# Kernel optimization log

Measured on AMD Instinct MI355X. Metric: run time of the kernel, lower is better.

## Reference

```python
import jax, jax.numpy as jnp
import numpy as np

N, B, E, D, DQ, H = 20000, 32, 320000, 128, 1024, 2
L = N // B  # 625 nodes per graph (equal-size graphs -> static max_node_num)
NUM_GNN_LAYERS = 3


def setup_inputs() -> dict:
    key = jax.random.key(0)
    ks = jax.random.split(key, 32)
    rn = lambda k, s, scale=1.0: jax.random.normal(k, s, jnp.float32) * scale
    w = lambda k, fi, fo: rn(k, (fi, fo), 1.0 / np.sqrt(fi))
    inp = {
        'x': rn(ks[0], (N, D)),
        'edge_attr': rn(ks[1], (E, D)),
        'u': rn(ks[2], (B, D)),
        'qa_attr': rn(ks[3], (B, DQ)),
        # edge MLP: cat(src,dest,edge_attr,u[eb]) = 4D -> hidden D -> D
        'W_e1': w(ks[4], 4 * D, D), 'b_e1': jnp.zeros((D,)),
        'W_e2': w(ks[5], D, D), 'b_e2': jnp.zeros((D,)),
        # weight mlp: cat(edge_attr, u[eb]) = 2D -> 1 (num_layers=1)
        'W_w': w(ks[6], 2 * D, 1), 'b_w': jnp.zeros((1,)),
        # message mlp: cat(x[row], edge_attr) = 2D -> D -> D
        'W_m1': w(ks[7], 2 * D, D), 'b_m1': jnp.zeros((D,)),
        'W_m2': w(ks[8], D, D), 'b_m2': jnp.zeros((D,)),
        # update mlp: cat(x, received, u[nb]) = 3D -> D -> D
        'W_u1': w(ks[9], 3 * D, D), 'b_u1': jnp.zeros((D,)),
        'W_u2': w(ks[10], D, D), 'b_u2': jnp.zeros((D,)),
        # multihead att-pool: q from qa_attr (DQ) -> H*dk; k,v from evidence (D) -> H*dk
        'W_q': w(ks[11], DQ, D), 'b_q': jnp.zeros((D,)),
        'W_k': w(ks[12], D, D), 'b_k': jnp.zeros((D,)),
        'W_v': w(ks[13], D, D), 'b_v': jnp.zeros((D,)),
        'edge_index': jax.random.randint(ks[14], (2, E), 0, N, dtype=jnp.int32),
        'node_batch': (jnp.arange(N, dtype=jnp.int32) // L).astype(jnp.int32),
        'num_of_nodes': jnp.full((B,), L, dtype=jnp.int32),
    }
    return inp


def _mlp2(h, W1, b1, W2, b2):
    return jax.nn.relu(h @ W1 + b1) @ W2 + b2


def _seg_softmax(logits, seg, num):
    m = jax.ops.segment_max(logits, seg, num_segments=num)
    e = jnp.exp(logits - m[seg])
    s = jax.ops.segment_sum(e, seg, num_segments=num)
    return e / s[seg]


def reference(x, edge_attr, u, qa_attr,
              W_e1, b_e1, W_e2, b_e2, W_w, b_w,
              W_m1, b_m1, W_m2, b_m2, W_u1, b_u1, W_u2, b_u2,
              W_q, b_q, W_k, b_k, W_v, b_v,
              edge_index, node_batch, num_of_nodes):
    row, col = edge_index[0], edge_index[1]
    edge_batch = node_batch[row]
    Bsz, Nn = u.shape[0], x.shape[0]
    Lm = Nn // Bsz  # static max_node_num (equal-size graphs)

    norm_w = None
    for _ in range(NUM_GNN_LAYERS):
        ue = u[edge_batch]  # [E, D]
        # EdgeModel: cat(src, dest, edge_attr, u[eb]) -> MLP -> new edge_attr
        new_edge = _mlp2(jnp.concatenate([x[row], x[col], edge_attr, ue], 1),
                         W_e1, b_e1, W_e2, b_e2)
        # edge weights from OLD edge_attr (per EdgeV1Model.forward)
        wts = jnp.concatenate([edge_attr, ue], 1) @ W_w + b_w  # [E,1]
        norm_w = _seg_softmax(wts[:, 0], edge_batch, Bsz)[:, None]  # [E,1]
        edge_attr = new_edge
        # NodeModel: message MLP, weighted scatter_mean over col, update MLP
        msg = _mlp2(jnp.concatenate([x[row], edge_attr], 1), W_m1, b_m1, W_m2, b_m2)
        summed = jax.ops.segment_sum(msg * norm_w, col, num_segments=Nn)
        cnt = jax.ops.segment_sum(jnp.ones((msg.shape[0],), msg.dtype), col, num_segments=Nn)
        received = summed / jnp.maximum(cnt, 1.0)[:, None]
        x = _mlp2(jnp.concatenate([x, received, u[node_batch]], 1),
                  W_u1, b_u1, W_u2, b_u2)

    pooled_edge = jax.ops.segment_sum(edge_attr * norm_w, edge_batch, num_segments=Bsz)  # [B,D]
    # evidence packing: equal graphs -> simple reshape, then exact GELU
    evidence = jax.nn.gelu(x.reshape(Bsz, Lm, -1), approximate=False)  # [B,L,D]
    mask = jnp.arange(Lm)[None, :] >= num_of_nodes[:, None]  # [B,L] True = masked

    # MultiheadAttPoolLayer
    dk = W_k.shape[1] // H
    q = (qa_attr @ W_q + b_q).reshape(Bsz, H, dk)
    k = (evidence @ W_k + b_k).reshape(Bsz, Lm, H, dk)
    v = (evidence @ W_v + b_v).reshape(Bsz, Lm, H, dk)
    scores = jnp.einsum('bhd,blhd->bhl', q, k) / jnp.sqrt(jnp.float32(dk))
    scores = jnp.where(mask[:, None, :], -1e30, scores)
    attn = jax.nn.softmax(scores, axis=-1)
    pooled_node = jnp.einsum('bhl,blhd->bhd', attn, v).reshape(Bsz, H * dk)  # [B,D]

    return jnp.concatenate([pooled_edge, pooled_node], 1)  # [B, 2D]
```

## Files before the change

### kernel.cpp

```cpp
#include <hip/hip_runtime.h>
#include <math.h>

typedef __bf16 bf16_t;
typedef bf16_t bf16x8 __attribute__((ext_vector_type(8)));
typedef bf16_t bf16x4 __attribute__((ext_vector_type(4)));
typedef bf16_t bf16x2 __attribute__((ext_vector_type(2)));
typedef float  f32x4  __attribute__((ext_vector_type(4)));

#define N_NODES 20000
#define NEDGE   320000
#define DIM     128
#define TP      136
#define EBLK    2500
#define FWAVES  10000
#define NBLK    625
#define GPRE    157
#define PBLK    512

#define FE1  0
#define FCE  49152
#define FM1  65536
#define FCM  81920
#define FU1  114688
#define FU2  163840
#define FK   180224
#define FV   196608
#define FWC  212992
#define WF_ELEMS 229376

__device__ __forceinline__ void acc_zero32(f32x4 acc[2][8]) {
  f32x4 z = {0.f, 0.f, 0.f, 0.f};
#pragma unroll
  for (int i = 0; i < 2; ++i)
#pragma unroll
    for (int j = 0; j < 8; ++j) acc[i][j] = z;
}

__device__ __forceinline__ void wstage_rows_bf(bf16_t* sA, const bf16_t* src, int rowreg, int lane) {
  int r = lane >> 1, h = lane & 1;
  int row = __shfl(rowreg, r);
  const bf16_t* sp = src + (size_t)row * DIM + h * 64;
  bf16_t* dp = sA + r * TP + h * 64;
#pragma unroll
  for (int i = 0; i < 8; ++i)
    *(uint4*)(dp + i * 8) = *(const uint4*)(sp + i * 8);
}

__device__ __forceinline__ void wstage_rows_f32(bf16_t* sA, const float* src, int rowreg, int lane) {
  int r = lane >> 1, h = lane & 1;
  int row = __shfl(rowreg, r);
  const float* sp = src + (size_t)row * DIM + h * 64;
  bf16_t* dp = sA + r * TP + h * 64;
#pragma unroll
  for (int i = 0; i < 8; ++i) {
    float4 f0 = *(const float4*)(sp + i * 8);
    float4 f1 = *(const float4*)(sp + i * 8 + 4);
    bf16x8 tv;
    tv[0]=(bf16_t)f0.x; tv[1]=(bf16_t)f0.y; tv[2]=(bf16_t)f0.z; tv[3]=(bf16_t)f0.w;
    tv[4]=(bf16_t)f1.x; tv[5]=(bf16_t)f1.y; tv[6]=(bf16_t)f1.z; tv[7]=(bf16_t)f1.w;
    *(bf16x8*)(dp + i * 8) = tv;
  }
}

__device__ __forceinline__ void wstage_seq_bf(bf16_t* sA, const bf16_t* src, int base, int lane) {
  int r = lane >> 1, h = lane & 1;
  const bf16_t* sp = src + (size_t)(base + r) * DIM + h * 64;
  bf16_t* dp = sA + r * TP + h * 64;
#pragma unroll
  for (int i = 0; i < 8; ++i)
    *(uint4*)(dp + i * 8) = *(const uint4*)(sp + i * 8);
}

__device__ __forceinline__ void wstage_seq_f32(bf16_t* sA, const float* src, int base, int lane) {
  int r = lane >> 1, h = lane & 1;
  const float* sp = src + (size_t)(base + r) * DIM + h * 64;
  bf16_t* dp = sA + r * TP + h * 64;
#pragma unroll
  for (int i = 0; i < 8; ++i) {
    float4 f0 = *(const float4*)(sp + i * 8);
    float4 f1 = *(const float4*)(sp + i * 8 + 4);
    bf16x8 tv;
    tv[0]=(bf16_t)f0.x; tv[1]=(bf16_t)f0.y; tv[2]=(bf16_t)f0.z; tv[3]=(bf16_t)f0.w;
    tv[4]=(bf16_t)f1.x; tv[5]=(bf16_t)f1.y; tv[6]=(bf16_t)f1.z; tv[7]=(bf16_t)f1.w;
    *(bf16x8*)(dp + i * 8) = tv;
  }
}

__device__ __forceinline__ void chunk_stage(bf16_t* ch, const bf16_t* __restrict__ src, int t) {
#pragma unroll
  for (int i = 0; i < 8; ++i) {
    int idx = (i * 256 + t) * 8;
    *(uint4*)(ch + idx) = *(const uint4*)(src + idx);
  }
}

__device__ __forceinline__ void wmfma_lds(const bf16_t* sA, const bf16_t* ch,
                                          int lane, int lm, int lq, f32x4 acc[2][8]) {
#pragma unroll
  for (int kk = 0; kk < 4; ++kk) {
    int ko = kk * 32 + lq * 8;
    bf16x8 a0 = *(const bf16x8*)(sA + lm * TP + ko);
    bf16x8 a1 = *(const bf16x8*)(sA + (16 + lm) * TP + ko);
    const bf16_t* wp = ch + (kk << 12) + (lane << 3);
#pragma unroll
    for (int ct = 0; ct < 8; ++ct) {
      bf16x8 bfr = *(const bf16x8*)(wp + (ct << 9));
      acc[0][ct] = __builtin_amdgcn_mfma_f32_16x16x32_bf16(a0, bfr, acc[0][ct], 0, 0, 0);
      acc[1][ct] = __builtin_amdgcn_mfma_f32_16x16x32_bf16(a1, bfr, acc[1][ct], 0, 0, 0);
    }
  }
}

__device__ __forceinline__ void wmfma_gk128(const bf16_t* sA, const bf16_t* __restrict__ Wf,
                                            int lane, int lm, int lq, f32x4 acc[2][8]) {
#pragma unroll
  for (int kk = 0; kk < 4; ++kk) {
    int ko = kk * 32 + lq * 8;
    bf16x8 a0 = *(const bf16x8*)(sA + lm * TP + ko);
    bf16x8 a1 = *(const bf16x8*)(sA + (16 + lm) * TP + ko);
    const bf16_t* wp = Wf + ((kk * 8) << 9) + (lane << 3);
#pragma unroll
    for (int ct = 0; ct < 8; ++ct) {
      bf16x8 bfr = *(const bf16x8*)(wp + (ct << 9));
      acc[0][ct] = __builtin_amdgcn_mfma_f32_16x16x32_bf16(a0, bfr, acc[0][ct], 0, 0, 0);
      acc[1][ct] = __builtin_amdgcn_mfma_f32_16x16x32_bf16(a1, bfr, acc[1][ct], 0, 0, 0);
    }
  }
}

__device__ __forceinline__ void merge_shfl(float& m, float& s, int width) {
  for (int k = 1; k < width; k <<= 1) {
    float m2 = __shfl_xor(m, k), s2 = __shfl_xor(s, k);
    float M = fmaxf(m, m2), ns = 0.f;
    if (m  > -1e29f) ns += s  * expf(m  - M);
    if (m2 > -1e29f) ns += s2 * expf(m2 - M);
    m = M; s = ns;
  }
}

__global__ void gn_xcvt(const float* x, bf16_t* xb) {
  int i = blockIdx.x * 256 + threadIdx.x;
  if (i < N_NODES * DIM / 4) {
    float4 f = ((const float4*)x)[i];
    bf16x4 o; o[0]=(bf16_t)f.x; o[1]=(bf16_t)f.y; o[2]=(bf16_t)f.z; o[3]=(bf16_t)f.w;
    *(bf16x4*)(xb + (size_t)i * 4) = o;
  }
}

__global__ void gn_wcomb(const float* Wm2, const float* Wu1, const float* We2,
                         const float* We1, const float* Wm1,
                         float* wc1, float* wce, float* wcm) {
  int idx = blockIdx.x * 256 + threadIdx.x;
  if (idx >= 16384) return;
  int i = idx >> 7, j = idx & 127;
  float acc = 0.f;
  if (blockIdx.y == 0) {
    for (int m = 0; m < 128; ++m) acc += Wm2[i * 128 + m] * Wu1[(128 + m) * 128 + j];
    wc1[idx] = acc;
  } else if (blockIdx.y == 1) {
    for (int m = 0; m < 128; ++m) acc += We2[i * 128 + m] * We1[(256 + m) * 128 + j];
    wce[idx] = acc;
  } else {
    for (int m = 0; m < 128; ++m) acc += We2[i * 128 + m] * Wm1[(128 + m) * 128 + j];
    wcm[idx] = acc;
  }
}

__global__ void gn_fragw(const float* We1, const float* Wce, const float* Wm1, const float* Wcm,
                         const float* Wm2, const float* Wu1, const float* Wu2,
                         const float* Wk, const float* Wv, const float* Wc1, bf16_t* WF) {
  int idx = blockIdx.x * 256 + threadIdx.x;
  if (idx >= WF_ELEMS) return;
  int seg = idx >> 14;
  const float* W; int kc;
  switch (seg) {
    case 0:  W = We1; kc = 0; break;
    case 1:  W = We1; kc = 1; break;
    case 2:  W = We1; kc = 2; break;
    case 3:  W = Wce; kc = 0; break;
    case 4:  W = Wm1; kc = 0; break;
    case 5:  W = Wcm; kc = 0; break;
    case 6:  W = Wm2; kc = 0; break;
    case 7:  W = Wu1; kc = 0; break;
    case 8:  W = Wu1; kc = 1; break;
    case 9:  W = Wu1; kc = 2; break;
    case 10: W = Wu2; kc = 0; break;
    case 11: W = Wk;  kc = 0; break;
    case 12: W = Wv;  kc = 0; break;
    default: W = Wc1; kc = 0; break;
  }
  int r = idx & 16383;
  int j = r & 7, lane = (r >> 3) & 63, ct = (r >> 9) & 7, kk = (r >> 12) & 3;
  int k = kc * 128 + kk * 32 + (lane >> 4) * 8 + j;
  int n = ct * 16 + (lane & 15);
  WF[idx] = (bf16_t)W[k * 128 + n];
}

__global__ void gn_uprep(const float* u, const float* We1, const float* be1,
                         const float* Ww, const float* bw,
                         const float* bm2, const float* Wu1,
                         const float* bm1, const float* be2,
                         const float* Wm1, const float* We2,
                         float* Rp0, float* Rp12, float* uw, float* uw2,
                         float* bm2u, float* bm1p, float* wv) {
  int t = threadIdx.x;
  for (int idx = blockIdx.x * 256 + t; idx < 32 * 128; idx += gridDim.x * 256) {
    int g = idx >> 7, c = idx & 127;
    float acc = be1[c];
    for (int k = 0; k < 128; ++k) acc += u[g * 128 + k] * We1[(384 + k) * 128 + c];
    float be12 = 0.f;
    for (int k = 0; k < 128; ++k) be12 += be2[k] * We1[(256 + k) * 128 + c];
    int tc = g * 128 + (c & 15) * 8 + (c >> 4);
    Rp0[tc] = acc;
    Rp12[tc] = acc + be12;
  }
  if (blockIdx.x == 0 && t < 32) {
    float acc = bw[0];
    for (int k = 0; k < 128; ++k) acc += u[t * 128 + k] * Ww[128 + k];
    float bsh = 0.f;
    for (int c = 0; c < 128; ++c) bsh += be2[c] * Ww[c];
    uw[t] = acc;
    uw2[t] = acc + bsh;
  }
  if (blockIdx.x == 1 && t < 128) {
    float a1 = 0.f, a2 = 0.f, a3 = 0.f;
    for (int k = 0; k < 128; ++k) {
      a1 += bm2[k] * Wu1[(128 + k) * 128 + t];
      a2 += be2[k] * Wm1[(128 + k) * 128 + t];
      a3 += We2[t * 128 + k] * Ww[k];
    }
    bm2u[t] = a1;
    bm1p[t] = bm1[t] + a2;
    wv[t] = a3;
  }
}

__global__ void gn_counti(const int* ei, int* cnti) {
  int e = blockIdx.x * 256 + threadIdx.x;
  if (e < NEDGE) atomicAdd(&cnti[ei[NEDGE + e]], 1);
}

__global__ void gn_scan(const int* cnti, int* off, int* curs) {
  __shared__ int part[256];
  int t = threadIdx.x;
  int base = t * 80;
  int lim = base + 80; if (lim > N_NODES) lim = N_NODES;
  int s = 0;
  for (int i = base; i < lim; ++i) s += cnti[i];
  part[t] = s;
  __syncthreads();
  for (int d = 1; d < 256; d <<= 1) {
    int add = (t >= d) ? part[t - d] : 0;
    __syncthreads();
    part[t] += add;
    __syncthreads();
  }
  int pfx = (t == 0) ? 0 : part[t - 1];
  for (int i = base; i < lim; ++i) {
    off[i] = pfx; curs[i] = pfx; pfx += cnti[i];
  }
  if (t == 0) off[N_NODES] = NEDGE;
}

__global__ void gn_eidx(const int* ei, int* curs, int* eidx) {
  int e = blockIdx.x * 256 + threadIdx.x;
  if (e < NEDGE) {
    int c = ei[NEDGE + e];
    int pos = atomicAdd(&curs[c], 1);
    eidx[pos] = e;
  }
}

__global__ void gn_q(const float* qa, const float* Wq, const float* bq, float* qb) {
  int b = blockIdx.x, t = threadIdx.x;
  int c = t & 127, half = t >> 7;
  const float* qrow = qa + b * 1024 + half * 512;
  float acc = 0.f;
  for (int k = 0; k < 512; ++k) acc += qrow[k] * Wq[(half * 512 + k) * 128 + c];
  __shared__ float red[256];
  red[t] = acc;
  __syncthreads();
  if (half == 0) qb[b * 128 + c] = red[c] + red[128 + c] + bq[c];
}

__global__ void gn_wl0(const float* ea, const float* Ww, const float* uw,
                       const int* ei, const int* nbat, float* wl, int* gb) {
  int t = threadIdx.x;
  int sub = t & 15, grp = t >> 4;
  for (int e = blockIdx.x * 16 + grp; e < NEDGE; e += gridDim.x * 16) {
    const float* er = ea + (size_t)e * DIM + sub * 8;
    float s = 0.f;
#pragma unroll
    for (int j = 0; j < 8; ++j) s += er[j] * Ww[sub * 8 + j];
#pragma unroll
    for (int m = 1; m < 16; m <<= 1) s += __shfl_xor(s, m);
    if (sub == 0) {
      int g = nbat[ei[e]];
      wl[e] = s + uw[g];
      gb[e] = g;
    }
  }
}

__global__ void gn_part0(const float* wl, const int* gb, float* pm, float* ps) {
  __shared__ float lv[128];
  __shared__ int   lgg[128];
  int t = threadIdx.x, blk = blockIdx.x, e0 = blk * 128;
  if (t < 128) { lv[t] = wl[e0 + t]; lgg[t] = gb[e0 + t]; }
  __syncthreads();
  int g = t >> 3, seg = t & 7;
  float m = -1e30f, s = 0.f;
  for (int i = seg * 16; i < seg * 16 + 16; ++i)
    if (lgg[i] == g) {
      float v = lv[i];
      if (v > m) { s = s * expf(m - v) + 1.f; m = v; }
      else s += expf(v - m);
    }
  merge_shfl(m, s, 8);
  if (seg == 0) { pm[g * FWAVES + blk] = m; ps[g * FWAVES + blk] = s; }
}

__global__ void gn_reduce_ms(const float* pm, const float* ps, float* mg, float* sg, int nb) {
  int g = blockIdx.x, t = threadIdx.x;
  __shared__ float red[256];
  float m = -1e30f;
  for (int i = t; i < nb; i += 256) m = fmaxf(m, pm[g * FWAVES + i]);
  red[t] = m; __syncthreads();
  for (int s2 = 128; s2 > 0; s2 >>= 1) { if (t < s2) red[t] = fmaxf(red[t], red[t + s2]); __syncthreads(); }
  m = red[0]; __syncthreads();
  float s = 0.f;
  for (int i = t; i < nb; i += 256) {
    float sb = ps[g * FWAVES + i];
    if (sb > 0.f) s += sb * expf(pm[g * FWAVES + i] - m);
  }
  red[t] = s; __syncthreads();
  for (int s2 = 128; s2 > 0; s2 >>= 1) { if (t < s2) red[t] += red[t + s2]; __syncthreads(); }
  if (t == 0) { mg[g] = m; sg[g] = red[0]; }
}

__global__ __launch_bounds__(256, 2) void gn_fused(
    const bf16_t* __restrict__ xb,
    const void* esrcv, int efirst,
    bf16_t* edst,
    const bf16_t* __restrict__ WF,
    const float* Rp, const float* UW2, const float* wv, const float* bm1p,
    const float* wl_cur, const float* mg, const float* sg,
    float* wl_next, float* pm, float* ps, int last,
    const int* ei, const int* gb, bf16_t* msg,
    const float* uu, const float* bu1, const int* nbat, float* pre,
    float* nwout) {
  __shared__ bf16_t chunk[16384];
  __shared__ bf16_t band[4][32 * TP];
  __shared__ float slwt[128];

  int t = threadIdx.x;
  int w = t >> 6, lane = t & 63;
  int lm = lane & 15, lq = lane >> 4;
  int blk = blockIdx.x;
  bf16_t* myband = band[w];

  if (blk >= EBLK) {
    int nb128 = blk - EBLK;
    int gb32 = nb128 * 4 + w;
    int lrow = 0, lgr = 0;
    if (lane < 32) {
      int node = gb32 * 32 + lane;
      if (node > N_NODES - 1) node = N_NODES - 1;
      lrow = node;
      lgr = nbat[node];
    }
    f32x4 acc[2][8];
    acc_zero32(acc);
    wstage_rows_bf(myband, xb, lrow, lane);
    chunk_stage(chunk, WF + FU1, t);
    __syncthreads();
    wmfma_lds(myband, chunk, lane, lm, lq, acc);
    __syncthreads();
    wstage_rows_f32(myband, uu, lgr, lane);
    chunk_stage(chunk, WF + FU1 + 32768, t);
    __syncthreads();
    wmfma_lds(myband, chunk, lane, lm, lq, acc);
    if (gb32 < NBLK) {
      float* pp = pre + (size_t)gb32 * 4096 + lane;
#pragma unroll
      for (int rt = 0; rt < 2; ++rt)
#pragma unroll
        for (int reg = 0; reg < 4; ++reg)
#pragma unroll
          for (int ct = 0; ct < 8; ++ct)
            pp[((rt * 32 + reg * 8 + ct) << 6)] = acc[rt][ct][reg] + bu1[ct * 16 + lm];
    }
    return;
  }

  int e0 = blk * 128;
  int ew0 = e0 + w * 32;
  int lrowr = 0, lcolr = 0, lgr = 0;
  float lnwr = 0.f;
  if (lane < 32) {
    int e = ew0 + lane;
    lrowr = ei[e];
    lcolr = ei[NEDGE + e];
    lgr = gb[e];
    lnwr = expf(wl_cur[e] - mg[lgr]) / sg[lgr];
    nwout[e] = lnwr;
  }

  f32x4 accE[2][8], accM[2][8];
  acc_zero32(accE);
  acc_zero32(accM);

  uint4 c0, c1, c2, c3, c4, c5, c6, c7;
#define CLOAD(SRC) { const uint4* _s = (const uint4*)(SRC) + t; \
  c0 = _s[0];    c1 = _s[256];  c2 = _s[512];  c3 = _s[768]; \
  c4 = _s[1024]; c5 = _s[1280]; c6 = _s[1536]; c7 = _s[1792]; }
#define CWRITE() { uint4* _d = (uint4*)chunk + t; \
  _d[0] = c0;    _d[256] = c1;  _d[512] = c2;  _d[768] = c3; \
  _d[1024] = c4; _d[1280] = c5; _d[1536] = c6; _d[1792] = c7; }

  CLOAD(WF + FE1);
  wstage_rows_bf(myband, xb, lrowr, lane);
  CWRITE();
  __syncthreads();

  CLOAD(WF + FM1);
  wmfma_lds(myband, chunk, lane, lm, lq, accE);
  __syncthreads();
  CWRITE();
  __syncthreads();

  CLOAD(WF + FE1 + 16384);
  wmfma_lds(myband, chunk, lane, lm, lq, accM);
  wstage_rows_bf(myband, xb, lcolr, lane);
  __syncthreads();
  CWRITE();
  __syncthreads();

  CLOAD(efirst ? (WF + FE1 + 32768) : (WF + FCE));
  wmfma_lds(myband, chunk, lane, lm, lq, accE);
  if (efirst) wstage_seq_f32(myband, (const float*)esrcv, ew0, lane);
  else        wstage_seq_bf (myband, (const bf16_t*)esrcv, ew0, lane);
  __syncthreads();
  CWRITE();
  __syncthreads();

  CLOAD(WF + FCM);
  wmfma_lds(myband, chunk, lane, lm, lq, accE);
  {
    float ww8[8];
#pragma unroll
    for (int ct = 0; ct < 8; ++ct) ww8[ct] = wv[ct * 16 + lm];
#pragma unroll
    for (int rt = 0; rt < 2; ++rt)
#pragma unroll
      for (int reg = 0; reg < 4; ++reg) {
        int row = rt * 16 + lq * 4 + reg;
        int g = __shfl(lgr, row);
        const float4* rp = (const float4*)(Rp + (size_t)g * 128 + lm * 8);
        float4 ra = rp[0], rb = rp[1];
        float rv[8] = {ra.x, ra.y, ra.z, ra.w, rb.x, rb.y, rb.z, rb.w};
        float lsum = 0.f;
#pragma unroll
        for (int ct = 0; ct < 8; ++ct) {
          int col = ct * 16 + lm;
          float v = fmaxf(accE[rt][ct][reg] + rv[ct], 0.f);
          myband[row * TP + col] = (bf16_t)v;
          lsum += v * ww8[ct];
        }
        if (!last) {
          lsum += __shfl_xor(lsum, 1);
          lsum += __shfl_xor(lsum, 2);
          lsum += __shfl_xor(lsum, 4);
          lsum += __shfl_xor(lsum, 8);
          if (lm == 0) {
            float v2 = lsum + UW2[g];
            wl_next[ew0 + row] = v2;
            slwt[w * 32 + row] = v2;
          }
        }
      }
    int r = lane >> 1, h = lane & 1;
    bf16_t* dp = edst + (size_t)(ew0 + r) * DIM + h * 64;
    const bf16_t* sp2 = myband + r * TP + h * 64;
#pragma unroll
    for (int i = 0; i < 8; ++i)
      *(uint4*)(dp + i * 8) = *(const uint4*)(sp2 + i * 8);
  }
  __syncthreads();
  CWRITE();
  __syncthreads();

  wmfma_lds(myband, chunk, lane, lm, lq, accM);
  {
    float bm18[8];
#pragma unroll
    for (int ct = 0; ct < 8; ++ct) bm18[ct] = bm1p[ct * 16 + lm];
#pragma unroll
    for (int rt = 0; rt < 2; ++rt)
#pragma unroll
      for (int reg = 0; reg < 4; ++reg) {
        int row = rt * 16 + lq * 4 + reg;
        float nwv = __shfl(lnwr, row);
#pragma unroll
        for (int ct = 0; ct < 8; ++ct) {
          int col = ct * 16 + lm;
          myband[row * TP + col] = (bf16_t)(fmaxf(accM[rt][ct][reg] + bm18[ct], 0.f) * nwv);
        }
      }
    int r = lane >> 1, h = lane & 1;
    bf16_t* dp = msg + (size_t)(ew0 + r) * DIM + h * 64;
    const bf16_t* sp2 = myband + r * TP + h * 64;
#pragma unroll
    for (int i = 0; i < 8; ++i)
      *(uint4*)(dp + i * 8) = *(const uint4*)(sp2 + i * 8);
  }

  if (!last) {
    int g = lane >> 1, seg = lane & 1;
    float m = -1e30f, s = 0.f;
    for (int i = seg * 16; i < seg * 16 + 16; ++i) {
      int gi = __shfl(lgr, i);
      if (gi == g) {
        float v = slwt[w * 32 + i];
        if (v > m) { s = s * expf(m - v) + 1.f; m = v; }
        else s += expf(v - m);
      }
    }
    merge_shfl(m, s, 2);
    if (seg == 0) { pm[g * FWAVES + blk * 4 + w] = m; ps[g * FWAVES + blk * 4 + w] = s; }
  }
#undef CLOAD
#undef CWRITE
}

__global__ __launch_bounds__(256) void gn_gather(
    const bf16_t* __restrict__ msg, const float* __restrict__ nw,
    const int* __restrict__ off, const int* __restrict__ eidx,
    bf16_t* recvb, float* rnw) {
  int w = threadIdx.x >> 6, lane = threadIdx.x & 63;
  int n = blockIdx.x * 4 + w;
  int o0 = off[n], o1 = off[n + 1];
  float a0 = 0.f, a1 = 0.f, snw = 0.f;
  int i = o0;
  for (; i + 3 < o1; i += 4) {
    int e0 = eidx[i], e1 = eidx[i + 1], e2 = eidx[i + 2], e3 = eidx[i + 3];
    bf16x2 v0 = *(const bf16x2*)(msg + (size_t)e0 * DIM + lane * 2);
    bf16x2 v1 = *(const bf16x2*)(msg + (size_t)e1 * DIM + lane * 2);
    bf16x2 v2 = *(const bf16x2*)(msg + (size_t)e2 * DIM + lane * 2);
    bf16x2 v3 = *(const bf16x2*)(msg + (size_t)e3 * DIM + lane * 2);
    a0 += (float)v0[0] + (float)v1[0] + (float)v2[0] + (float)v3[0];
    a1 += (float)v0[1] + (float)v1[1] + (float)v2[1] + (float)v3[1];
    snw += nw[e0] + nw[e1] + nw[e2] + nw[e3];
  }
  for (; i < o1; ++i) {
    int e = eidx[i];
    bf16x2 v = *(const bf16x2*)(msg + (size_t)e * DIM + lane * 2);
    a0 += (float)v[0];
    a1 += (float)v[1];
    snw += nw[e];
  }
  float ic = 1.f / fmaxf((float)(o1 - o0), 1.f);
  bf16x2 o; o[0] = (bf16_t)(a0 * ic); o[1] = (bf16_t)(a1 * ic);
  *(bf16x2*)(recvb + (size_t)n * DIM + lane * 2) = o;
  if (lane == 0) rnw[n] = snw * ic;
}

__global__ __launch_bounds__(64, 3) void gn_node(
    bf16_t* xdst, const bf16_t* recvb, const float* rnw, const float* pre,
    const bf16_t* __restrict__ WF, const float* bu2, const float* bm2u) {
  __shared__ bf16_t sA[32 * TP];

  int lane = threadIdx.x;
  int nb = blockIdx.x;
  int n0 = nb * 32;
  int lm = lane & 15, lq = lane >> 4;

  float rnwreg = 0.f;
  if (lane < 32) rnwreg = rnw[n0 + lane];

  wstage_seq_bf(sA, recvb, n0, lane);

  f32x4 acc[2][8];
  acc_zero32(acc);
  wmfma_gk128(sA, WF + FWC, lane, lm, lq, acc);

  const float* pp = pre + (size_t)nb * 4096 + lane;
  float bm2u8[8];
#pragma unroll
  for (int ct = 0; ct < 8; ++ct) bm2u8[ct] = bm2u[ct * 16 + lm];
#pragma unroll
  for (int rt = 0; rt < 2; ++rt)
#pragma unroll
    for (int reg = 0; reg < 4; ++reg) {
      int row = rt * 16 + lq * 4 + reg;
      float rv = __shfl(rnwreg, row);
#pragma unroll
      for (int ct = 0; ct < 8; ++ct) {
        int col = ct * 16 + lm;
        sA[row * TP + col] = (bf16_t)fmaxf(
            acc[rt][ct][reg] + rv * bm2u8[ct] + pp[((rt * 32 + reg * 8 + ct) << 6)], 0.f);
      }
    }
  acc_zero32(acc);
  wmfma_gk128(sA, WF + FU2, lane, lm, lq, acc);

  {
    float bu28[8];
#pragma unroll
    for (int ct = 0; ct < 8; ++ct) bu28[ct] = bu2[ct * 16 + lm];
#pragma unroll
    for (int rt = 0; rt < 2; ++rt)
#pragma unroll
      for (int reg = 0; reg < 4; ++reg) {
        int row = rt * 16 + lq * 4 + reg;
        bf16_t* dr = xdst + (size_t)(n0 + row) * DIM;
#pragma unroll
        for (int ct = 0; ct < 8; ++ct) {
          int col = ct * 16 + lm;
          dr[col] = (bf16_t)(acc[rt][ct][reg] + bu28[ct]);
        }
      }
  }
}

__global__ __launch_bounds__(64, 3) void gn_ev(
    const bf16_t* xsrc, const bf16_t* __restrict__ WF,
    const float* bk, const float* bv, float* kb, float* vb) {
  __shared__ bf16_t sA[32 * TP];

  int lane = threadIdx.x;
  int n0 = blockIdx.x * 32;
  int sel = blockIdx.y;
  const bf16_t* Wf = WF + (sel ? FV : FK);
  const float* bias = sel ? bv : bk;
  float* dst = sel ? vb : kb;
  int lm = lane & 15, lq = lane >> 4;

  {
    int r = lane >> 1, h = lane & 1;
    const bf16_t* sp = xsrc + (size_t)(n0 + r) * DIM + h * 64;
    bf16_t* dp = sA + r * TP + h * 64;
#pragma unroll
    for (int i = 0; i < 8; ++i) {
      uint4 v = *(const uint4*)(sp + i * 8);
      bf16_t tmp[8];
      *(uint4*)tmp = v;
      bf16x8 tv;
#pragma unroll
      for (int j = 0; j < 8; ++j) {
        float f = (float)tmp[j];
        tv[j] = (bf16_t)(0.5f * f * (1.f + erff(f * 0.70710678118654752f)));
      }
      *(bf16x8*)(dp + i * 8) = tv;
    }
  }

  f32x4 acc[2][8];
  acc_zero32(acc);
  wmfma_gk128(sA, Wf, lane, lm, lq, acc);

  {
    float b8[8];
#pragma unroll
    for (int ct = 0; ct < 8; ++ct) b8[ct] = bias[ct * 16 + lm];
#pragma unroll
    for (int rt = 0; rt < 2; ++rt)
#pragma unroll
      for (int reg = 0; reg < 4; ++reg) {
        int row = rt * 16 + lq * 4 + reg;
        float* dr = dst + (size_t)(n0 + row) * DIM;
#pragma unroll
        for (int ct = 0; ct < 8; ++ct) {
          int col = ct * 16 + lm;
          dr[col] = acc[rt][ct][reg] + b8[ct];
        }
      }
  }
}

__global__ __launch_bounds__(256, 2) void gn_pooled_edge(
    const bf16_t* __restrict__ he, const float* __restrict__ nw,
    const int* __restrict__ gb, float* pep, float* pepn) {
  __shared__ float loc[4][4096];
  __shared__ float nws[4][32];
  int t = threadIdx.x;
  int lane = t & 63, w = t >> 6;
  float* myloc = loc[w];
  for (int i = lane; i < 4096; i += 64) myloc[i] = 0.f;
  if (lane < 32) nws[w][lane] = 0.f;

  int wid = blockIdx.x * 4 + w;
  int c0 = lane * 2;
  for (int e = wid; e < NEDGE; e += PBLK * 4) {
    int g = gb[e];
    float nwt = nw[e];
    bf16x2 v = *(const bf16x2*)(he + (size_t)e * DIM + c0);
    float* a = myloc + g * 128 + c0;
    float2 cur = *(float2*)a;
    cur.x += (float)v[0] * nwt;
    cur.y += (float)v[1] * nwt;
    *(float2*)a = cur;
    if (lane == 0) nws[w][g] += nwt;
  }
  __syncthreads();
  float* pp = pep + (size_t)blockIdx.x * 4096;
  for (int i = t; i < 4096; i += 256)
    pp[i] = loc[0][i] + loc[1][i] + loc[2][i] + loc[3][i];
  if (t < 32)
    pepn[blockIdx.x * 32 + t] = nws[0][t] + nws[1][t] + nws[2][t] + nws[3][t];
}

__global__ __launch_bounds__(1024) void gn_att(
    const float* qb, const float* kb, const float* vb, const int* non, float* out) {
  int b = blockIdx.x >> 1, h = blockIdx.x & 1, t = threadIdx.x;
  __shared__ float qv[64];
  __shared__ float sc[625];
  __shared__ float red[1024];
  if (t < 64) qv[t] = qb[b * 128 + h * 64 + t];
  __syncthreads();
  int nn = non[b];
  const float4* qv4 = (const float4*)qv;
  for (int l = t; l < 625; l += 1024) {
    float acc = 0.f;
    const float4* kr = (const float4*)(kb + ((size_t)(b * 625 + l)) * DIM + h * 64);
#pragma unroll
    for (int d2 = 0; d2 < 16; ++d2) {
      float4 kv = kr[d2];
      float4 qq = qv4[d2];
      acc += qq.x * kv.x + qq.y * kv.y + qq.z * kv.z + qq.w * kv.w;
    }
    sc[l] = (l < nn) ? acc * 0.125f : -1e30f;
  }
  __syncthreads();
  float m = -1e30f;
  for (int l = t; l < 625; l += 1024) m = fmaxf(m, sc[l]);
  red[t] = m; __syncthreads();
  for (int s2 = 512; s2 > 0; s2 >>= 1) { if (t < s2) red[t] = fmaxf(red[t], red[t + s2]); __syncthreads(); }
  m = red[0]; __syncthreads();
  float ssum = 0.f;
  for (int l = t; l < 625; l += 1024) { float e = expf(sc[l] - m); sc[l] = e; ssum += e; }
  red[t] = ssum; __syncthreads();
  for (int s2 = 512; s2 > 0; s2 >>= 1) { if (t < s2) red[t] += red[t + s2]; __syncthreads(); }
  float inv = 1.f / red[0];
  __syncthreads();
  int d = t & 63, seg = t >> 6;
  float acc = 0.f;
  for (int l = seg; l < 625; l += 16) acc += sc[l] * vb[((size_t)(b * 625 + l)) * DIM + h * 64 + d];
  red[t] = acc; __syncthreads();
  if (t < 64) {
    float v = 0.f;
#pragma unroll
    for (int s = 0; s < 16; ++s) v += red[s * 64 + t];
    out[b * 256 + 128 + h * 64 + d] = v * inv;
  }
}

__global__ void gn_fin1(const float* pep, const float* pepn, float* spool, float* nwg) {
  int i = blockIdx.x * 256 + threadIdx.x;
  float s = 0.f;
#pragma unroll 8
  for (int blk = 0; blk < PBLK; ++blk) s += pep[(size_t)blk * 4096 + i];
  spool[i] = s;
  if (i < 32) {
    float sn = 0.f;
    for (int blk = 0; blk < PBLK; ++blk) sn += pepn[blk * 32 + i];
    nwg[i] = sn;
  }
}

__global__ void gn_fin2(const float* spool, const float* nwg, const float* We2,
                        const float* be2, float* out) {
  int i = blockIdx.x * 256 + threadIdx.x;
  int b = i >> 7, c = i & 127;
  float acc = nwg[b] * be2[c];
  for (int k = 0; k < 128; ++k) acc += spool[b * 128 + k] * We2[k * 128 + c];
  out[b * 256 + c] = acc;
}

extern "C" void kernel_launch(void* const* d_in, const int* in_sizes, int n_in,
                              void* d_out, int out_size, void* d_ws, size_t ws_size,
                              hipStream_t stream) {
  const float* x   = (const float*)d_in[0];
  const float* ea  = (const float*)d_in[1];
  const float* u   = (const float*)d_in[2];
  const float* qa  = (const float*)d_in[3];
  const float* We1 = (const float*)d_in[4];
  const float* be1 = (const float*)d_in[5];
  const float* We2 = (const float*)d_in[6];
  const float* be2 = (const float*)d_in[7];
  const float* Ww  = (const float*)d_in[8];
  const float* bw  = (const float*)d_in[9];
  const float* Wm1 = (const float*)d_in[10];
  const float* bm1 = (const float*)d_in[11];
  const float* Wm2 = (const float*)d_in[12];
  const float* bm2 = (const float*)d_in[13];
  const float* Wu1 = (const float*)d_in[14];
  const float* bu1 = (const float*)d_in[15];
  const float* Wu2 = (const float*)d_in[16];
  const float* bu2 = (const float*)d_in[17];
  const float* Wq  = (const float*)d_in[18];
  const float* bq  = (const float*)d_in[19];
  const float* Wk  = (const float*)d_in[20];
  const float* bk  = (const float*)d_in[21];
  const float* Wv  = (const float*)d_in[22];
  const float* bv  = (const float*)d_in[23];
  const int* ei   = (const int*)d_in[24];
  const int* nbat = (const int*)d_in[25];
  const int* non  = (const int*)d_in[26];
  float* out = (float*)d_out;

  char* p = (char*)d_ws;
  auto alloc = [&](size_t bytes) { char* r = p; p += (bytes + 255) & ~(size_t)255; return r; };
  bf16_t* EB    = (bf16_t*)alloc((size_t)NEDGE * DIM * 2);
  bf16_t* XB    = (bf16_t*)alloc((size_t)N_NODES * DIM * 2);
  bf16_t* XB0   = (bf16_t*)alloc((size_t)N_NODES * DIM * 2);
  bf16_t* MSG   = (bf16_t*)alloc((size_t)NEDGE * DIM * 2);
  bf16_t* RECVB = (bf16_t*)alloc((size_t)N_NODES * DIM * 2);
  int*   CNTI = (int*)alloc((size_t)N_NODES * 4);
  int*   OFF  = (int*)alloc((size_t)(N_NODES + 1) * 4);
  int*   CURS = (int*)alloc((size_t)N_NODES * 4);
  int*   EIDX = (int*)alloc((size_t)NEDGE * 4);
  float* WL   = (float*)alloc((size_t)NEDGE * 4);
  float* WLn  = (float*)alloc((size_t)NEDGE * 4);
  float* NW   = (float*)alloc((size_t)NEDGE * 4);
  float* RNW  = (float*)alloc((size_t)N_NODES * 4);
  int*   GB   = (int*)alloc((size_t)NEDGE * 4);
  float* PM   = (float*)alloc((size_t)32 * FWAVES * 4);
  float* PS   = (float*)alloc((size_t)32 * FWAVES * 4);
  float* MG   = (float*)alloc(32 * 4);
  float* SG   = (float*)alloc(32 * 4);
  float* RP0  = (float*)alloc(32 * 128 * 4);
  float* RP12 = (float*)alloc(32 * 128 * 4);
  float* UW   = (float*)alloc(32 * 4);
  float* UW2  = (float*)alloc(32 * 4);
  float* WC1  = (float*)alloc(16384 * 4);
  float* WCE  = (float*)alloc(16384 * 4);
  float* WCM  = (float*)alloc(16384 * 4);
  float* BM2U = (float*)alloc(128 * 4);
  float* BM1P = (float*)alloc(128 * 4);
  float* WVV  = (float*)alloc(128 * 4);
  bf16_t* WF  = (bf16_t*)alloc((size_t)WF_ELEMS * 2);
  float* QB   = (float*)alloc(32 * 128 * 4);
  float* KB   = (float*)alloc((size_t)N_NODES * DIM * 4);
  float* VB   = (float*)alloc((size_t)N_NODES * DIM * 4);
  float* PEP  = (float*)alloc((size_t)PBLK * 4096 * 4);
  float* PEPN = (float*)alloc((size_t)PBLK * 32 * 4);
  float* SPOOL= (float*)alloc(4096 * 4);
  float* NWG  = (float*)alloc(32 * 4);
  float* PRE  = (float*)alloc((size_t)N_NODES * DIM * 4);

  hipMemsetAsync(CNTI, 0, (size_t)N_NODES * 4, stream);

  gn_xcvt<<<(N_NODES * DIM / 4 + 255) / 256, 256, 0, stream>>>(x, XB0);
  gn_wcomb<<<dim3(64, 3), 256, 0, stream>>>(Wm2, Wu1, We2, We1, Wm1, WC1, WCE, WCM);
  gn_fragw<<<(WF_ELEMS + 255) / 256, 256, 0, stream>>>(We1, WCE, Wm1, WCM, Wm2, Wu1, Wu2, Wk, Wv, WC1, WF);
  gn_uprep<<<16, 256, 0, stream>>>(u, We1, be1, Ww, bw, bm2, Wu1, bm1, be2, Wm1, We2,
                                   RP0, RP12, UW, UW2, BM2U, BM1P, WVV);
  gn_counti<<<1250, 256, 0, stream>>>(ei, CNTI);
  gn_scan<<<1, 256, 0, stream>>>(CNTI, OFF, CURS);
  gn_eidx<<<1250, 256, 0, stream>>>(ei, CURS, EIDX);
  gn_q<<<32, 256, 0, stream>>>(qa, Wq, bq, QB);
  gn_wl0<<<2500, 256, 0, stream>>>(ea, Ww, UW, ei, nbat, WL, GB);
  gn_part0<<<EBLK, 256, 0, stream>>>(WL, GB, PM, PS);

  for (int layer = 0; layer < 3; ++layer) {
    int first = (layer == 0) ? 1 : 0;
    int last = (layer == 2) ? 1 : 0;
    const bf16_t* xs = first ? XB0 : XB;
    const void* es = first ? (const void*)ea : (const void*)EB;
    const float* rp = first ? RP0 : RP12;
    float* cur = (layer == 1) ? WLn : WL;
    float* nxt = (layer == 1) ? WL : WLn;
    gn_reduce_ms<<<32, 256, 0, stream>>>(PM, PS, MG, SG, first ? EBLK : FWAVES);
    gn_fused<<<EBLK + GPRE, 256, 0, stream>>>(xs, es, first, EB, WF, rp, UW2, WVV, BM1P,
                                              cur, MG, SG, nxt, PM, PS, last, ei, GB, MSG,
                                              u, bu1, nbat, PRE, NW);
    gn_gather<<<5000, 256, 0, stream>>>(MSG, NW, OFF, EIDX, RECVB, RNW);
    gn_node<<<NBLK, 64, 0, stream>>>(XB, RECVB, RNW, PRE, WF, bu2, BM2U);
  }

  gn_pooled_edge<<<PBLK, 256, 0, stream>>>(EB, NW, GB, PEP, PEPN);
  gn_ev<<<dim3(NBLK, 2), 64, 0, stream>>>(XB, WF, bk, bv, KB, VB);
  gn_att<<<64, 1024, 0, stream>>>(QB, KB, VB, non, out);
  gn_fin1<<<16, 256, 0, stream>>>(PEP, PEPN, SPOOL, NWG);
  gn_fin2<<<16, 256, 0, stream>>>(SPOOL, NWG, We2, be2, out);
}
```

Baseline: 1.259 ms.

## Widen fused edge kernel to 12 waves per block sharing staged weight chunks

The fused edge/message kernel now runs 768-thread blocks (12 waves, 384 edges) instead of 256-thread blocks. Each staged weight chunk in LDS is therefore shared by three times as many waves, cutting weight-staging traffic per edge. The separate edge and message accumulators are merged into one, with the message MLP moved after the edge MLP, which lowers register pressure enough to allow larger blocks. Smaller changes vectorise the wl0 loads and widen the softmax-stat reduction to 1024 threads. The cost is one resident block per CU, more barrier-heavy synchronisation across 12 waves, and a partial tail block.

```diff
diff --git a/kernel.cpp b/kernel.cpp
--- a/kernel.cpp
+++ b/kernel.cpp
@@ -14,7 +14,9 @@
 #define EBLK    2500
 #define FWAVES  10000
 #define NBLK    625
-#define GPRE    157
+#define EWBLK   384
+#define EBLK2   834
+#define PREB    53
 #define PBLK    512
 
 #define FE1  0
@@ -83,14 +85,6 @@
     tv[0]=(bf16_t)f0.x; tv[1]=(bf16_t)f0.y; tv[2]=(bf16_t)f0.z; tv[3]=(bf16_t)f0.w;
     tv[4]=(bf16_t)f1.x; tv[5]=(bf16_t)f1.y; tv[6]=(bf16_t)f1.z; tv[7]=(bf16_t)f1.w;
     *(bf16x8*)(dp + i * 8) = tv;
-  }
-}
-
-__device__ __forceinline__ void chunk_stage(bf16_t* ch, const bf16_t* __restrict__ src, int t) {
-#pragma unroll
-  for (int i = 0; i < 8; ++i) {
-    int idx = (i * 256 + t) * 8;
-    *(uint4*)(ch + idx) = *(const uint4*)(src + idx);
   }
 }
 
@@ -288,10 +282,11 @@
   int t = threadIdx.x;
   int sub = t & 15, grp = t >> 4;
   for (int e = blockIdx.x * 16 + grp; e < NEDGE; e += gridDim.x * 16) {
-    const float* er = ea + (size_t)e * DIM + sub * 8;
-    float s = 0.f;
-#pragma unroll
-    for (int j = 0; j < 8; ++j) s += er[j] * Ww[sub * 8 + j];
+    const float4* er4 = (const float4*)(ea + (size_t)e * DIM + sub * 8);
+    float4 va = er4[0], vb = er4[1];
+    const float* wp = Ww + sub * 8;
+    float s = va.x * wp[0] + va.y * wp[1] + va.z * wp[2] + va.w * wp[3]
+            + vb.x * wp[4] + vb.y * wp[5] + vb.z * wp[6] + vb.w * wp[7];
 #pragma unroll
     for (int m = 1; m < 16; m <<= 1) s += __shfl_xor(s, m);
     if (sub == 0) {
@@ -320,25 +315,26 @@
   if (seg == 0) { pm[g * FWAVES + blk] = m; ps[g * FWAVES + blk] = s; }
 }
 
-__global__ void gn_reduce_ms(const float* pm, const float* ps, float* mg, float* sg, int nb) {
+__global__ __launch_bounds__(1024) void gn_reduce_ms(
+    const float* pm, const float* ps, float* mg, float* sg, int nb) {
   int g = blockIdx.x, t = threadIdx.x;
-  __shared__ float red[256];
+  __shared__ float red[1024];
   float m = -1e30f;
-  for (int i = t; i < nb; i += 256) m = fmaxf(m, pm[g * FWAVES + i]);
+  for (int i = t; i < nb; i += 1024) m = fmaxf(m, pm[g * FWAVES + i]);
   red[t] = m; __syncthreads();
-  for (int s2 = 128; s2 > 0; s2 >>= 1) { if (t < s2) red[t] = fmaxf(red[t], red[t + s2]); __syncthreads(); }
+  for (int s2 = 512; s2 > 0; s2 >>= 1) { if (t < s2) red[t] = fmaxf(red[t], red[t + s2]); __syncthreads(); }
   m = red[0]; __syncthreads();
   float s = 0.f;
-  for (int i = t; i < nb; i += 256) {
+  for (int i = t; i < nb; i += 1024) {
     float sb = ps[g * FWAVES + i];
     if (sb > 0.f) s += sb * expf(pm[g * FWAVES + i] - m);
   }
   red[t] = s; __syncthreads();
-  for (int s2 = 128; s2 > 0; s2 >>= 1) { if (t < s2) red[t] += red[t + s2]; __syncthreads(); }
+  for (int s2 = 512; s2 > 0; s2 >>= 1) { if (t < s2) red[t] += red[t + s2]; __syncthreads(); }
   if (t == 0) { mg[g] = m; sg[g] = red[0]; }
 }
 
-__global__ __launch_bounds__(256, 2) void gn_fused(
+__global__ __launch_bounds__(768, 1) void gn_fused(
     const bf16_t* __restrict__ xb,
     const void* esrcv, int efirst,
     bf16_t* edst,
@@ -350,8 +346,8 @@
     const float* uu, const float* bu1, const int* nbat, float* pre,
     float* nwout) {
   __shared__ bf16_t chunk[16384];
-  __shared__ bf16_t band[4][32 * TP];
-  __shared__ float slwt[128];
+  __shared__ bf16_t band[12][32 * TP];
+  __shared__ float slwt[384];
 
   int t = threadIdx.x;
   int w = t >> 6, lane = t & 63;
@@ -359,28 +355,37 @@
   int blk = blockIdx.x;
   bf16_t* myband = band[w];
 
-  if (blk >= EBLK) {
-    int nb128 = blk - EBLK;
-    int gb32 = nb128 * 4 + w;
+  uint4 c0, c1, c2, c3;
+#define CLOAD(SRC) if (t < 512) { const uint4* _s = (const uint4*)(SRC) + t; \
+  c0 = _s[0]; c1 = _s[512]; c2 = _s[1024]; c3 = _s[1536]; }
+#define CWRITE() if (t < 512) { uint4* _d = (uint4*)chunk + t; \
+  _d[0] = c0; _d[512] = c1; _d[1024] = c2; _d[1536] = c3; }
+
+  if (blk >= EBLK2) {
+    int gb32 = (blk - EBLK2) * 12 + w;
+    int act = (gb32 < NBLK);
     int lrow = 0, lgr = 0;
-    if (lane < 32) {
+    if (act && lane < 32) {
       int node = gb32 * 32 + lane;
-      if (node > N_NODES - 1) node = N_NODES - 1;
       lrow = node;
       lgr = nbat[node];
     }
     f32x4 acc[2][8];
     acc_zero32(acc);
-    wstage_rows_bf(myband, xb, lrow, lane);
-    chunk_stage(chunk, WF + FU1, t);
+    CLOAD(WF + FU1);
+    if (act) wstage_rows_bf(myband, xb, lrow, lane);
+    CWRITE();
     __syncthreads();
-    wmfma_lds(myband, chunk, lane, lm, lq, acc);
+    CLOAD(WF + FU1 + 32768);
+    if (act) {
+      wmfma_lds(myband, chunk, lane, lm, lq, acc);
+      wstage_rows_f32(myband, uu, lgr, lane);
+    }
     __syncthreads();
-    wstage_rows_f32(myband, uu, lgr, lane);
-    chunk_stage(chunk, WF + FU1 + 32768, t);
+    CWRITE();
     __syncthreads();
-    wmfma_lds(myband, chunk, lane, lm, lq, acc);
-    if (gb32 < NBLK) {
+    if (act) {
+      wmfma_lds(myband, chunk, lane, lm, lq, acc);
       float* pp = pre + (size_t)gb32 * 4096 + lane;
 #pragma unroll
       for (int rt = 0; rt < 2; ++rt)
@@ -393,11 +398,11 @@
     return;
   }
 
-  int e0 = blk * 128;
-  int ew0 = e0 + w * 32;
+  int ew0 = blk * EWBLK + w * 32;
+  int act = (ew0 < NEDGE);
   int lrowr = 0, lcolr = 0, lgr = 0;
   float lnwr = 0.f;
-  if (lane < 32) {
+  if (act && lane < 32) {
     int e = ew0 + lane;
     lrowr = ei[e];
     lcolr = ei[NEDGE + e];
@@ -406,47 +411,36 @@
     nwout[e] = lnwr;
   }
 
-  f32x4 accE[2][8], accM[2][8];
-  acc_zero32(accE);
-  acc_zero32(accM);
-
-  uint4 c0, c1, c2, c3, c4, c5, c6, c7;
-#define CLOAD(SRC) { const uint4* _s = (const uint4*)(SRC) + t; \
-  c0 = _s[0];    c1 = _s[256];  c2 = _s[512];  c3 = _s[768]; \
-  c4 = _s[1024]; c5 = _s[1280]; c6 = _s[1536]; c7 = _s[1792]; }
-#define CWRITE() { uint4* _d = (uint4*)chunk + t; \
-  _d[0] = c0;    _d[256] = c1;  _d[512] = c2;  _d[768] = c3; \
-  _d[1024] = c4; _d[1280] = c5; _d[1536] = c6; _d[1792] = c7; }
+  f32x4 acc[2][8];
+  acc_zero32(acc);
 
   CLOAD(WF + FE1);
-  wstage_rows_bf(myband, xb, lrowr, lane);
+  if (act) wstage_rows_bf(myband, xb, lrowr, lane);
   CWRITE();
   __syncthreads();
 
-  CLOAD(WF + FM1);
-  wmfma_lds(myband, chunk, lane, lm, lq, accE);
+  CLOAD(WF + FE1 + 16384);
+  if (act) {
+    wmfma_lds(myband, chunk, lane, lm, lq, acc);
+    wstage_rows_bf(myband, xb, lcolr, lane);
+  }
   __syncthreads();
   CWRITE();
   __syncthreads();
 
-  CLOAD(WF + FE1 + 16384);
-  wmfma_lds(myband, chunk, lane, lm, lq, accM);
-  wstage_rows_bf(myband, xb, lcolr, lane);
+  CLOAD(efirst ? (WF + FE1 + 32768) : (WF + FCE));
+  if (act) {
+    wmfma_lds(myband, chunk, lane, lm, lq, acc);
+    if (efirst) wstage_seq_f32(myband, (const float*)esrcv, ew0, lane);
+    else        wstage_seq_bf (myband, (const bf16_t*)esrcv, ew0, lane);
+  }
   __syncthreads();
   CWRITE();
   __syncthreads();
 
-  CLOAD(efirst ? (WF + FE1 + 32768) : (WF + FCE));
-  wmfma_lds(myband, chunk, lane, lm, lq, accE);
-  if (efirst) wstage_seq_f32(myband, (const float*)esrcv, ew0, lane);
-  else        wstage_seq_bf (myband, (const bf16_t*)esrcv, ew0, lane);
-  __syncthreads();
-  CWRITE();
-  __syncthreads();
-
   CLOAD(WF + FCM);
-  wmfma_lds(myband, chunk, lane, lm, lq, accE);
-  {
+  if (act) {
+    wmfma_lds(myband, chunk, lane, lm, lq, acc);
     float ww8[8];
 #pragma unroll
     for (int ct = 0; ct < 8; ++ct) ww8[ct] = wv[ct * 16 + lm];
@@ -463,7 +457,7 @@
 #pragma unroll
         for (int ct = 0; ct < 8; ++ct) {
           int col = ct * 16 + lm;
-          float v = fmaxf(accE[rt][ct][reg] + rv[ct], 0.f);
+          float v = fmaxf(acc[rt][ct][reg] + rv[ct], 0.f);
           myband[row * TP + col] = (bf16_t)v;
           lsum += v * ww8[ct];
         }
@@ -489,9 +483,19 @@
   __syncthreads();
   CWRITE();
   __syncthreads();
-
-  wmfma_lds(myband, chunk, lane, lm, lq, accM);
-  {
+  acc_zero32(acc);
+
+  CLOAD(WF + FM1);
+  if (act) {
+    wmfma_lds(myband, chunk, lane, lm, lq, acc);
+    wstage_rows_bf(myband, xb, lrowr, lane);
+  }
+  __syncthreads();
+  CWRITE();
+  __syncthreads();
+
+  if (act) {
+    wmfma_lds(myband, chunk, lane, lm, lq, acc);
     float bm18[8];
 #pragma unroll
     for (int ct = 0; ct < 8; ++ct) bm18[ct] = bm1p[ct * 16 + lm];
@@ -504,7 +508,7 @@
 #pragma unroll
         for (int ct = 0; ct < 8; ++ct) {
           int col = ct * 16 + lm;
-          myband[row * TP + col] = (bf16_t)(fmaxf(accM[rt][ct][reg] + bm18[ct], 0.f) * nwv);
+          myband[row * TP + col] = (bf16_t)(fmaxf(acc[rt][ct][reg] + bm18[ct], 0.f) * nwv);
         }
       }
     int r = lane >> 1, h = lane & 1;
@@ -513,21 +517,21 @@
 #pragma unroll
     for (int i = 0; i < 8; ++i)
       *(uint4*)(dp + i * 8) = *(const uint4*)(sp2 + i * 8);
-  }
-
-  if (!last) {
-    int g = lane >> 1, seg = lane & 1;
-    float m = -1e30f, s = 0.f;
-    for (int i = seg * 16; i < seg * 16 + 16; ++i) {
-      int gi = __shfl(lgr, i);
-      if (gi == g) {
-        float v = slwt[w * 32 + i];
-        if (v > m) { s = s * expf(m - v) + 1.f; m = v; }
-        else s += expf(v - m);
+
+    if (!last) {
+      int g = lane >> 1, seg = lane & 1;
+      float m = -1e30f, s = 0.f;
+      for (int i = seg * 16; i < seg * 16 + 16; ++i) {
+        int gi = __shfl(lgr, i);
+        if (gi == g) {
+          float v = slwt[w * 32 + i];
+          if (v > m) { s = s * expf(m - v) + 1.f; m = v; }
+          else s += expf(v - m);
+        }
       }
-    }
-    merge_shfl(m, s, 2);
-    if (seg == 0) { pm[g * FWAVES + blk * 4 + w] = m; ps[g * FWAVES + blk * 4 + w] = s; }
+      merge_shfl(m, s, 2);
+      if (seg == 0) { pm[g * FWAVES + blk * 12 + w] = m; ps[g * FWAVES + blk * 12 + w] = s; }
+    }
   }
 #undef CLOAD
 #undef CWRITE
@@ -871,10 +875,10 @@
     const float* rp = first ? RP0 : RP12;
     float* cur = (layer == 1) ? WLn : WL;
     float* nxt = (layer == 1) ? WL : WLn;
-    gn_reduce_ms<<<32, 256, 0, stream>>>(PM, PS, MG, SG, first ? EBLK : FWAVES);
-    gn_fused<<<EBLK + GPRE, 256, 0, stream>>>(xs, es, first, EB, WF, rp, UW2, WVV, BM1P,
-                                              cur, MG, SG, nxt, PM, PS, last, ei, GB, MSG,
-                                              u, bu1, nbat, PRE, NW);
+    gn_reduce_ms<<<32, 1024, 0, stream>>>(PM, PS, MG, SG, first ? EBLK : FWAVES);
+    gn_fused<<<EBLK2 + PREB, 768, 0, stream>>>(xs, es, first, EB, WF, rp, UW2, WVV, BM1P,
+                                               cur, MG, SG, nxt, PM, PS, last, ei, GB, MSG,
+                                               u, bu1, nbat, PRE, NW);
     gn_gather<<<5000, 256, 0, stream>>>(MSG, NW, OFF, EIDX, RECVB, RNW);
     gn_node<<<NBLK, 64, 0, stream>>>(XB, RECVB, RNW, PRE, WF, bu2, BM2U);
   }
```

After: 1.279 ms. Within noise of the previous version (+1.6%).
